# Kernel tuning notes

Hardware: AMD Instinct MI355X
Metric: run time of the kernel (lower is better)

Reference implementation:

```python
import jax, jax.numpy as jnp
import numpy as np
from jax import lax

B, C, NH, H, W = 2, 64, 8, 256, 256
HID = int(C * 2.66)  # 170, GDFN hidden channels


def conv1x1(x, w):
    # x: [b,c,h,w], w: [o,c] (1x1 conv, no bias)
    return jnp.einsum('bchw,oc->bohw', x, w)


def dwconv3(x, w):
    # depthwise 3x3, SAME padding; w: [ch,1,3,3]
    return lax.conv_general_dilated(
        x, w, window_strides=(1, 1), padding='SAME',
        feature_group_count=x.shape[1],
        dimension_numbers=('NCHW', 'OIHW', 'NCHW'))


def ln_ch(x, w, b, eps=1e-5):
    # LayerNorm over channel dim (torch does LN on [b,hw,c] then transposes back)
    mu = jnp.mean(x, axis=1, keepdims=True)
    var = jnp.mean((x - mu) ** 2, axis=1, keepdims=True)
    return (x - mu) / jnp.sqrt(var + eps) * w[None, :, None, None] + b[None, :, None, None]


def l2norm(x, eps=1e-12):
    # F.normalize(dim=-1): x / max(||x||_2, eps)
    n = jnp.sqrt(jnp.sum(x * x, axis=-1, keepdims=True))
    return x / jnp.maximum(n, eps)


def setup_inputs() -> dict:
    key = jax.random.key(0)
    ks = jax.random.split(key, 8)
    s = 0.02
    return dict(
        x=jax.random.normal(ks[0], (B, C, H, W), jnp.float32),
        y=jax.random.normal(ks[1], (B, C, H, W), jnp.float32),
        ln11_w=jnp.ones((C,), jnp.float32), ln11_b=jnp.zeros((C,), jnp.float32),
        ln12_w=jnp.ones((C,), jnp.float32), ln12_b=jnp.zeros((C,), jnp.float32),
        ln2_w=jnp.ones((C,), jnp.float32), ln2_b=jnp.zeros((C,), jnp.float32),
        qkv_w=jax.random.normal(ks[2], (3 * C, C), jnp.float32) * s,
        qkv_dw=jax.random.normal(ks[3], (3 * C, 1, 3, 3), jnp.float32) * s,
        temperature=jnp.ones((1, NH, 1, 1), jnp.float32),
        gdfn_in_w=jax.random.normal(ks[4], (2 * HID, C), jnp.float32) * s,
        gdfn_dw=jax.random.normal(ks[5], (2 * HID, 1, 3, 3), jnp.float32) * s,
        gdfn_out_w=jax.random.normal(ks[6], (C, HID), jnp.float32) * s,
    )


def _block(x, y, ln11_w, ln11_b, ln12_w, ln12_b, ln2_w, ln2_b,
           qkv_w, qkv_dw, temperature, gdfn_in_w, gdfn_dw, gdfn_out_w):
    b, c, h, w = x.shape
    xn = ln_ch(x, ln11_w, ln11_b)
    yn = ln_ch(y, ln12_w, ln12_b)

    def qkv_heads(z):
        t = dwconv3(conv1x1(z, qkv_w), qkv_dw)
        q, k, v = jnp.split(t, 3, axis=1)
        r = lambda a: a.reshape(b, NH, c // NH, h * w)
        return r(q), r(k), r(v)

    q, k, v = qkv_heads(xn)
    q1, k1, v1 = qkv_heads(yn)
    q, k, q1, k1 = l2norm(q), l2norm(k), l2norm(q1), l2norm(k1)

    # channel attention: [b,nh,c/nh,c/nh]; only cross_feature is used by the block
    attn_du = jax.nn.softmax(jnp.einsum('bhcn,bhdn->bhcd', q1, k) * temperature, axis=-1)
    attn_ud = jax.nn.softmax(jnp.einsum('bhcn,bhdn->bhcd', q, k1) * temperature, axis=-1)
    cross = (jnp.einsum('bhcd,bhdn->bhcn', attn_du, v) +
             jnp.einsum('bhcd,bhdn->bhcn', attn_ud, v1)).reshape(b, c, h, w)

    x = x + cross

    # GDFN
    xn2 = ln_ch(x, ln2_w, ln2_b)
    t = dwconv3(conv1x1(xn2, gdfn_in_w), gdfn_dw)
    x1, x2 = jnp.split(t, 2, axis=1)
    x = x + conv1x1(jax.nn.gelu(x1, approximate=False) * x2, gdfn_out_w)
    return x


def reference(x, y, ln11_w, ln11_b, ln12_w, ln12_b, ln2_w, ln2_b,
              qkv_w, qkv_dw, temperature, gdfn_in_w, gdfn_dw, gdfn_out_w):
    return _block(x, y, ln11_w, ln11_b, ln12_w, ln12_b, ln2_w, ln2_b,
                  qkv_w, qkv_dw, temperature, gdfn_in_w, gdfn_dw, gdfn_out_w)
```

## Files before the change

### kernel.cpp

```cpp
#include <hip/hip_runtime.h>
#include <hip/hip_bf16.h>
#include <math.h>

#define HWn 65536
#define Hh 256
#define Wd 256
#define Bb 2
#define Cc 64
#define NHh 8
#define HIDc 170
#define PXN 131072

typedef __hip_bfloat16 bf16;
typedef __attribute__((ext_vector_type(8))) short short8;
typedef __attribute__((ext_vector_type(4))) short s16x4;
typedef __attribute__((ext_vector_type(4))) float f32x4;

__device__ inline float b2f(short u) {
    unsigned int x = ((unsigned int)(unsigned short)u) << 16;
    return __uint_as_float(x);
}
__device__ inline short f2b(float f) {
    __hip_bfloat16 h = __float2bfloat16(f);
    return *reinterpret_cast<short*>(&h);
}
__device__ __forceinline__ void zero8(short8& v) {
#pragma unroll
    for (int e = 0; e < 8; e++) v[e] = 0;
}
__device__ __forceinline__ float rfl(float x) {
    return __uint_as_float(__builtin_amdgcn_readfirstlane(__float_as_uint(x)));
}
__device__ __forceinline__ float gelu_f(float x) {
    float z = fabsf(x) * 0.70710678118654752f;
    float tt = __builtin_amdgcn_rcpf(fmaf(0.3275911f, z, 1.f));
    float p = tt * fmaf(tt, fmaf(tt, fmaf(tt, fmaf(tt, 1.061405429f, -1.453152027f),
                                          1.421413741f), -0.284496736f), 0.254829592f);
    float e = __expf(-z * z);
    float er = fmaf(-p, e, 1.f);
    er = copysignf(er, x);
    return 0.5f * x * (1.f + er);
}

__device__ __forceinline__ void dw_row_f(const bf16* __restrict__ base, int y, int t,
                                         const float* wv, float acc[8]) {
#pragma unroll
    for (int e = 0; e < 8; e++) acc[e] = 0.f;
#pragma unroll
    for (int dy = 0; dy < 3; dy++) {
        int ys = y + dy - 1;
        if (ys < 0 || ys >= 256) continue;
        const bf16* rp = base + (size_t)ys * 2048 + (size_t)t * 8;
        short8 c8 = *reinterpret_cast<const short8*>(rp);
        short8 l8, r8;
        if (t > 0) l8 = *reinterpret_cast<const short8*>(rp - 8); else zero8(l8);
        if (t < 255) r8 = *reinterpret_cast<const short8*>(rp + 8); else zero8(r8);
#pragma unroll
        for (int e = 0; e < 8; e++)
            acc[e] += wv[e * 9 + dy * 3] * b2f(l8[e]) +
                      wv[e * 9 + dy * 3 + 1] * b2f(c8[e]) +
                      wv[e * 9 + dy * 3 + 2] * b2f(r8[e]);
    }
}

__global__ void zero_k(float* p, int n) {
    for (int i = threadIdx.x; i < n; i += 256) p[i] = 0.f;
}

__global__ __launch_bounds__(256, 2)
void ln_px(const float* __restrict__ x, const float* __restrict__ y,
           const float* __restrict__ w1, const float* __restrict__ b1,
           const float* __restrict__ w2, const float* __restrict__ b2,
           bf16* __restrict__ outx, bf16* __restrict__ outy) {
    const float* src = blockIdx.y ? y : x;
    const float* w = blockIdx.y ? w2 : w1;
    const float* bia = blockIdx.y ? b2 : b1;
    bf16* out = blockIdx.y ? outy : outx;
    int idx = blockIdx.x * 256 + threadIdx.x;
    int b = idx >> 16, p = idx & 65535;
    const float* xp = src + (size_t)b * 64 * HWn + p;
    float f[64];
    float s = 0.f;
#pragma unroll
    for (int c = 0; c < 64; c++) { f[c] = xp[(size_t)c * HWn]; s += f[c]; }
    float mu = s * (1.f / 64.f);
    float s2 = 0.f;
#pragma unroll
    for (int c = 0; c < 64; c++) { float d = f[c] - mu; s2 += d * d; }
    float inv = rsqrtf(s2 * (1.f / 64.f) + 1e-5f);
#pragma unroll
    for (int c8 = 0; c8 < 8; c8++) {
        short8 o;
#pragma unroll
        for (int e = 0; e < 8; e++) {
            int c = c8 * 8 + e;
            o[e] = f2b((f[c] - mu) * inv * w[c] + bia[c]);
        }
        *reinterpret_cast<short8*>(out + ((size_t)c8 * PXN + idx) * 8) = o;
    }
}

__global__ __launch_bounds__(256)
void conv1x1_mfma(const bf16* __restrict__ inA, const bf16* __restrict__ inB,
                  const float* __restrict__ w, int nstrips, int remap,
                  bf16* __restrict__ outA, bf16* __restrict__ outB) {
    const bf16* in = blockIdx.y ? inB : inA;
    bf16* out = blockIdx.y ? outB : outA;
    int lane = threadIdx.x & 63, wid = threadIdx.x >> 6;
    int r16 = lane & 15, grp = lane >> 4;
    size_t px0 = (size_t)blockIdx.x * 64;
    const bf16* bp0 = in + ((size_t)grp * PXN + px0 + r16) * 8;
    const bf16* bp1 = in + (((size_t)grp + 4) * PXN + px0 + r16) * 8;
    short8 b0[4], b1[4];
#pragma unroll
    for (int s = 0; s < 4; s++) {
        b0[s] = *reinterpret_cast<const short8*>(bp0 + s * 128);
        b1[s] = *reinterpret_cast<const short8*>(bp1 + s * 128);
    }
    for (int si = wid; si < nstrips; si += 4) {
        int co = si * 16 + r16;
        int row = co;
        if (remap) row = co < 170 ? co : (co >= 176 && co < 346 ? co - 6 : -1);
        short8 a0, a1;
        if (row >= 0) {
            const float* wr = w + (size_t)row * 64 + grp * 8;
#pragma unroll
            for (int e = 0; e < 8; e++) { a0[e] = f2b(wr[e]); a1[e] = f2b(wr[32 + e]); }
        } else {
            zero8(a0); zero8(a1);
        }
        int ochunk = si * 2 + (grp >> 1);
        int osub = (grp & 1) * 4;
#pragma unroll
        for (int s = 0; s < 4; s++) {
            f32x4 acc = {0.f, 0.f, 0.f, 0.f};
            acc = __builtin_amdgcn_mfma_f32_16x16x32_bf16(a0, b0[s], acc, 0, 0, 0);
            acc = __builtin_amdgcn_mfma_f32_16x16x32_bf16(a1, b1[s], acc, 0, 0, 0);
            size_t px = px0 + s * 16 + r16;
            s16x4 o;
#pragma unroll
            for (int j = 0; j < 4; j++) o[j] = f2b(acc[j]);
            *reinterpret_cast<s16x4*>(out + ((size_t)ochunk * PXN + px) * 8 + osub) = o;
        }
    }
}

__global__ __launch_bounds__(256, 4)
void dwconv_span(const bf16* __restrict__ inx, const bf16* __restrict__ iny,
                 const float* __restrict__ w, int c0,
                 bf16* __restrict__ outx, bf16* __restrict__ outy) {
    int cid = blockIdx.x >> 7;
    int rb = blockIdx.x & 127;
    int chunk = c0 + cid;
    const bf16* in = blockIdx.y ? iny : inx;
    bf16* out = blockIdx.y ? outy : outx;
    int t = threadIdx.x;
    float wv[72];
#pragma unroll
    for (int i = 0; i < 72; i++) wv[i] = w[chunk * 72 + i];
    int b = rb >> 6;
    const bf16* base = in + ((size_t)chunk * PXN + (size_t)b * 65536) * 8;
    bf16* obase = out + ((size_t)cid * PXN + (size_t)b * 65536) * 8;
#pragma unroll
    for (int r = 0; r < 4; r++) {
        int y = (rb * 4 + r) & 255;
        float acc[8];
        dw_row_f(base, y, t, wv, acc);
        short8 o;
#pragma unroll
        for (int e = 0; e < 8; e++) o[e] = f2b(acc[e]);
        *reinterpret_cast<short8*>(obase + ((size_t)y * 256 + t) * 8) = o;
    }
}

__global__ __launch_bounds__(256, 2)
void attn_dots_px(const bf16* __restrict__ qkx, const bf16* __restrict__ qky,
                  float* __restrict__ G, float* __restrict__ NA,
                  float* __restrict__ NB) {
    int which = blockIdx.z;
    int bh = blockIdx.y;
    int b = bh >> 3, h = bh & 7;
    const bf16* Aq = (which == 0 ? qky : qkx) + ((size_t)h * PXN + (size_t)b * 65536) * 8;
    const bf16* Bk = (which == 0 ? qkx : qky) + (((size_t)8 + h) * PXN + (size_t)b * 65536) * 8;
    float acc[8][8], na[8], nb[8];
#pragma unroll
    for (int c = 0; c < 8; c++) {
        na[c] = 0.f; nb[c] = 0.f;
#pragma unroll
        for (int d = 0; d < 8; d++) acc[c][d] = 0.f;
    }
    int per = 65536 / gridDim.x;
    int n0 = blockIdx.x * per;
    for (int n = n0 + threadIdx.x; n < n0 + per; n += 256) {
        short8 q8 = *reinterpret_cast<const short8*>(Aq + (size_t)n * 8);
        short8 k8 = *reinterpret_cast<const short8*>(Bk + (size_t)n * 8);
        float av[8], bv[8];
#pragma unroll
        for (int i = 0; i < 8; i++) { av[i] = b2f(q8[i]); bv[i] = b2f(k8[i]); }
#pragma unroll
        for (int c = 0; c < 8; c++) na[c] = fmaf(av[c], av[c], na[c]);
#pragma unroll
        for (int d = 0; d < 8; d++) nb[d] = fmaf(bv[d], bv[d], nb[d]);
#pragma unroll
        for (int c = 0; c < 8; c++)
#pragma unroll
            for (int d = 0; d < 8; d++) acc[c][d] = fmaf(av[c], bv[d], acc[c][d]);
    }
    size_t gbase = (((size_t)which * Bb + b) * 8 + h);
    float* Gp = G + gbase * 64;
#pragma unroll
    for (int c = 0; c < 8; c++)
#pragma unroll
        for (int d = 0; d < 8; d++) {
            float s = acc[c][d];
#pragma unroll
            for (int m = 1; m < 64; m <<= 1) s += __shfl_xor(s, m);
            if ((threadIdx.x & 63) == 0) atomicAdd(&Gp[c * 8 + d], s);
        }
#pragma unroll
    for (int c = 0; c < 8; c++) {
        float s = na[c];
#pragma unroll
        for (int m = 1; m < 64; m <<= 1) s += __shfl_xor(s, m);
        if ((threadIdx.x & 63) == 0) atomicAdd(&NA[gbase * 8 + c], s);
        float s2 = nb[c];
#pragma unroll
        for (int m = 1; m < 64; m <<= 1) s2 += __shfl_xor(s2, m);
        if ((threadIdx.x & 63) == 0) atomicAdd(&NB[gbase * 8 + c], s2);
    }
}

__global__ __launch_bounds__(256, 2)
void cross_ln2_px(const float* __restrict__ x, const bf16* __restrict__ vx,
                  const bf16* __restrict__ vy, const float* __restrict__ G,
                  const float* __restrict__ NA, const float* __restrict__ NB,
                  const float* __restrict__ temp,
                  const float* __restrict__ ln2w, const float* __restrict__ ln2b,
                  float* __restrict__ out, bf16* __restrict__ xn2) {
    int idx = blockIdx.x * 256 + threadIdx.x;
    int b = idx >> 16, p = idx & 65535;
    __shared__ float a1[512], a2[512];
    int t = threadIdx.x;
    if (t < 128) {
        int which = t >> 6, h = (t >> 3) & 7, c = t & 7;
        size_t gbase = (((size_t)which * Bb + b) * 8 + h);
        const float* Gp = G + gbase * 64 + c * 8;
        float an = fmaxf(sqrtf(NA[gbase * 8 + c]), 1e-12f);
        float tm = temp[h];
        float vals[8];
        float mx = -1e30f;
#pragma unroll
        for (int d = 0; d < 8; d++) {
            float bn = fmaxf(sqrtf(NB[gbase * 8 + d]), 1e-12f);
            float v = Gp[d] / (an * bn) * tm;
            vals[d] = v;
            mx = fmaxf(mx, v);
        }
        float se = 0.f;
#pragma unroll
        for (int d = 0; d < 8; d++) { vals[d] = expf(vals[d] - mx); se += vals[d]; }
        float inv = 1.f / se;
        float* ap = (which ? a2 : a1) + h * 64 + c * 8;
#pragma unroll
        for (int d = 0; d < 8; d++) ap[d] = vals[d] * inv;
    }
    __syncthreads();
    float o[64];
    const float* xp = x + (size_t)b * 64 * HWn + p;
#pragma unroll
    for (int c = 0; c < 64; c++) o[c] = xp[(size_t)c * HWn];
#pragma unroll
    for (int h = 0; h < 8; h++) {
        short8 v8 = *reinterpret_cast<const short8*>(vx + ((size_t)h * PXN + idx) * 8);
        short8 w8 = *reinterpret_cast<const short8*>(vy + ((size_t)h * PXN + idx) * 8);
        float v[8], v1[8];
#pragma unroll
        for (int d = 0; d < 8; d++) { v[d] = b2f(v8[d]); v1[d] = b2f(w8[d]); }
#pragma unroll
        for (int ci = 0; ci < 8; ci++) {
            float s = 0.f;
            const float* r1 = a1 + h * 64 + ci * 8;
            const float* r2 = a2 + h * 64 + ci * 8;
#pragma unroll
            for (int d = 0; d < 8; d++) s += r1[d] * v[d] + r2[d] * v1[d];
            o[h * 8 + ci] += s;
        }
    }
    float* op = out + (size_t)b * 64 * HWn + p;
    float s = 0.f;
#pragma unroll
    for (int c = 0; c < 64; c++) { op[(size_t)c * HWn] = o[c]; s += o[c]; }
    float mu = s * (1.f / 64.f);
    float s2 = 0.f;
#pragma unroll
    for (int c = 0; c < 64; c++) { float d = o[c] - mu; s2 += d * d; }
    float inv = rsqrtf(s2 * (1.f / 64.f) + 1e-5f);
#pragma unroll
    for (int c8 = 0; c8 < 8; c8++) {
        short8 o8;
#pragma unroll
        for (int e = 0; e < 8; e++) {
            int c = c8 * 8 + e;
            o8[e] = f2b((o[c] - mu) * inv * ln2w[c] + ln2b[c]);
        }
        *reinterpret_cast<short8*>(xn2 + ((size_t)c8 * PXN + idx) * 8) = o8;
    }
}

__global__ __launch_bounds__(256, 3)
void dwconv_gate(const bf16* __restrict__ g, const float* __restrict__ w,
                 bf16* __restrict__ tout) {
    int c = blockIdx.x >> 7;
    int rb = blockIdx.x & 127;
    int t = threadIdx.x;
    int b = rb >> 6;
    float wv[72];
#pragma unroll
    for (int i = 0; i < 72; i++)
        wv[i] = (c * 8 + i / 9 < 170) ? rfl(w[c * 72 + i]) : 0.f;
    const bf16* base1 = g + ((size_t)c * PXN + (size_t)b * 65536) * 8;
    float a1r[4][8];
#pragma unroll
    for (int r = 0; r < 4; r++) {
        int y = (rb * 4 + r) & 255;
        dw_row_f(base1, y, t, wv, a1r[r]);
    }
#pragma unroll
    for (int i = 0; i < 72; i++)
        wv[i] = (c * 8 + i / 9 < 170) ? rfl(w[(170 + c * 8) * 9 + i]) : 0.f;
    const bf16* base2 = g + (((size_t)22 + c) * PXN + (size_t)b * 65536) * 8;
    bf16* obase = tout + ((size_t)c * PXN + (size_t)b * 65536) * 8;
#pragma unroll
    for (int r = 0; r < 4; r++) {
        int y = (rb * 4 + r) & 255;
        float a2[8];
        dw_row_f(base2, y, t, wv, a2);
        short8 o;
#pragma unroll
        for (int e = 0; e < 8; e++)
            o[e] = f2b(gelu_f(a1r[r][e]) * a2[e]);
        *reinterpret_cast<short8*>(obase + ((size_t)y * 256 + t) * 8) = o;
    }
}

__global__ __launch_bounds__(256, 4)
void gdfn_out_mfma(const bf16* __restrict__ t, const float* __restrict__ wout,
                   float* __restrict__ out) {
    int lane = threadIdx.x & 63, wid = threadIdx.x >> 6;
    int r16 = lane & 15, grp = lane >> 4;
    size_t px0 = (size_t)blockIdx.x * 64;
    int co = wid * 16 + r16;
    short8 af[6];
#pragma unroll
    for (int kc = 0; kc < 6; kc++) {
#pragma unroll
        for (int e = 0; e < 8; e++) {
            int k = kc * 32 + grp * 8 + e;
            af[kc][e] = (k < 170) ? f2b(wout[(size_t)co * 170 + k]) : (short)0;
        }
    }
#pragma unroll
    for (int s = 0; s < 4; s++) {
        size_t px = px0 + s * 16 + r16;
        f32x4 acc = {0.f, 0.f, 0.f, 0.f};
#pragma unroll
        for (int kc = 0; kc < 6; kc++) {
            int cidx = kc * 4 + grp;
            short8 bv;
            if (cidx < 22) bv = *reinterpret_cast<const short8*>(t + ((size_t)cidx * PXN + px) * 8);
            else zero8(bv);
            acc = __builtin_amdgcn_mfma_f32_16x16x32_bf16(af[kc], bv, acc, 0, 0, 0);
        }
        int b = (int)(px >> 16);
        int p = (int)(px & 65535);
        float* op = out + (size_t)b * 64 * HWn + (size_t)(wid * 16 + grp * 4) * HWn + p;
#pragma unroll
        for (int j = 0; j < 4; j++) op[(size_t)j * HWn] += acc[j];
    }
}

extern "C" void kernel_launch(void* const* d_in, const int* in_sizes, int n_in,
                              void* d_out, int out_size, void* d_ws, size_t ws_size,
                              hipStream_t stream) {
    const float* x = (const float*)d_in[0];
    const float* y = (const float*)d_in[1];
    const float* ln11_w = (const float*)d_in[2];
    const float* ln11_b = (const float*)d_in[3];
    const float* ln12_w = (const float*)d_in[4];
    const float* ln12_b = (const float*)d_in[5];
    const float* ln2_w = (const float*)d_in[6];
    const float* ln2_b = (const float*)d_in[7];
    const float* qkv_w = (const float*)d_in[8];
    const float* qkv_dw = (const float*)d_in[9];
    const float* temp = (const float*)d_in[10];
    const float* gdfn_in_w = (const float*)d_in[11];
    const float* gdfn_dw = (const float*)d_in[12];
    const float* gdfn_out_w = (const float*)d_in[13];
    float* out = (float*)d_out;

    char* wsb = (char*)d_ws;
    float* G = (float*)wsb;
    float* NA = G + 2048;
    float* NB = NA + 256;
    bf16* hp = (bf16*)(wsb + 18944);
    bf16* xn   = hp;
    bf16* yn   = hp + (size_t)8388608;
    bf16* qkx  = hp;
    bf16* tx   = hp + (size_t)16777216;
    bf16* ty   = hp + (size_t)41943040;
    bf16* qky  = hp + (size_t)67108864;
    bf16* vx   = hp + (size_t)83886080;
    bf16* vy   = hp + (size_t)92274688;
    bf16* g    = hp + (size_t)16777216;
    bf16* t    = hp + (size_t)67108864;
    bf16* xn2  = hp;

    zero_k<<<1, 256, 0, stream>>>(G, 2560);

    ln_px<<<dim3(512, 2), 256, 0, stream>>>(x, y, ln11_w, ln11_b, ln12_w, ln12_b, xn, yn);

    conv1x1_mfma<<<dim3(2048, 2), 256, 0, stream>>>(xn, yn, qkv_w, 12, 0, tx, ty);

    dwconv_span<<<dim3(16 * 128, 2), 256, 0, stream>>>(tx, ty, qkv_dw, 0, qkx, qky);
    dwconv_span<<<dim3(8 * 128, 2), 256, 0, stream>>>(tx, ty, qkv_dw, 16, vx, vy);

    attn_dots_px<<<dim3(16, 16, 2), 256, 0, stream>>>(qkx, qky, G, NA, NB);

    cross_ln2_px<<<512, 256, 0, stream>>>(x, vx, vy, G, NA, NB, temp, ln2_w, ln2_b, out, xn2);

    conv1x1_mfma<<<dim3(2048, 1), 256, 0, stream>>>(xn2, xn2, gdfn_in_w, 22, 1, g, g);
    dwconv_gate<<<22 * 128, 256, 0, stream>>>(g, gdfn_dw, t);
    gdfn_out_mfma<<<2048, 256, 0, stream>>>(t, gdfn_out_w, out);
}
```

Before: 306.5 us.

## Store residual as bf16 and pack dwconv math into float2 ops

The residual after cross attention is now written as bf16 in the blocked channel layout instead of fp32 NCHW to the output, and the final GDFN projection reads it back and writes the output once rather than doing a read-modify-write. The depthwise convolutions unpack bf16 pairs into float2 vectors so the compiler can use packed FMA, and the two qkv dwconv launches are merged into one. This cuts fp32 residual traffic and instruction count, but rounds the residual to bf16, which may reduce accuracy.

```diff
diff --git a/kernel.cpp b/kernel.cpp
--- a/kernel.cpp
+++ b/kernel.cpp
@@ -15,6 +15,8 @@
 typedef __attribute__((ext_vector_type(8))) short short8;
 typedef __attribute__((ext_vector_type(4))) short s16x4;
 typedef __attribute__((ext_vector_type(4))) float f32x4;
+typedef __attribute__((ext_vector_type(2))) float f32x2;
+typedef __attribute__((ext_vector_type(4))) unsigned int u32x4;
 
 __device__ inline float b2f(short u) {
     unsigned int x = ((unsigned int)(unsigned short)u) << 16;
@@ -30,6 +32,12 @@
 }
 __device__ __forceinline__ float rfl(float x) {
     return __uint_as_float(__builtin_amdgcn_readfirstlane(__float_as_uint(x)));
+}
+__device__ __forceinline__ f32x2 bp2f(unsigned int d) {
+    f32x2 r;
+    r.x = __uint_as_float(d << 16);
+    r.y = __uint_as_float(d & 0xffff0000u);
+    return r;
 }
 __device__ __forceinline__ float gelu_f(float x) {
     float z = fabsf(x) * 0.70710678118654752f;
@@ -42,24 +50,30 @@
     return 0.5f * x * (1.f + er);
 }
 
-__device__ __forceinline__ void dw_row_f(const bf16* __restrict__ base, int y, int t,
-                                         const float* wv, float acc[8]) {
-#pragma unroll
-    for (int e = 0; e < 8; e++) acc[e] = 0.f;
+__device__ __forceinline__ void dw_row_p(const bf16* __restrict__ base, int y, int t,
+                                         const f32x2* wp, f32x2 acc[4]) {
+#pragma unroll
+    for (int p = 0; p < 4; p++) { acc[p].x = 0.f; acc[p].y = 0.f; }
 #pragma unroll
     for (int dy = 0; dy < 3; dy++) {
         int ys = y + dy - 1;
         if (ys < 0 || ys >= 256) continue;
         const bf16* rp = base + (size_t)ys * 2048 + (size_t)t * 8;
-        short8 c8 = *reinterpret_cast<const short8*>(rp);
-        short8 l8, r8;
-        if (t > 0) l8 = *reinterpret_cast<const short8*>(rp - 8); else zero8(l8);
-        if (t < 255) r8 = *reinterpret_cast<const short8*>(rp + 8); else zero8(r8);
-#pragma unroll
-        for (int e = 0; e < 8; e++)
-            acc[e] += wv[e * 9 + dy * 3] * b2f(l8[e]) +
-                      wv[e * 9 + dy * 3 + 1] * b2f(c8[e]) +
-                      wv[e * 9 + dy * 3 + 2] * b2f(r8[e]);
+        u32x4 c4 = *reinterpret_cast<const u32x4*>(rp);
+        u32x4 l4, r4;
+        if (t > 0) l4 = *reinterpret_cast<const u32x4*>(rp - 8);
+        else { l4.x = 0; l4.y = 0; l4.z = 0; l4.w = 0; }
+        if (t < 255) r4 = *reinterpret_cast<const u32x4*>(rp + 8);
+        else { r4.x = 0; r4.y = 0; r4.z = 0; r4.w = 0; }
+#pragma unroll
+        for (int p = 0; p < 4; p++) {
+            f32x2 fl = bp2f(l4[p]);
+            f32x2 fc = bp2f(c4[p]);
+            f32x2 fr = bp2f(r4[p]);
+            acc[p] += wp[(dy * 3 + 0) * 4 + p] * fl;
+            acc[p] += wp[(dy * 3 + 1) * 4 + p] * fc;
+            acc[p] += wp[(dy * 3 + 2) * 4 + p] * fr;
+        }
     }
 }
 
@@ -147,28 +161,36 @@
 
 __global__ __launch_bounds__(256, 4)
 void dwconv_span(const bf16* __restrict__ inx, const bf16* __restrict__ iny,
-                 const float* __restrict__ w, int c0,
-                 bf16* __restrict__ outx, bf16* __restrict__ outy) {
+                 const float* __restrict__ w,
+                 bf16* __restrict__ qkx, bf16* __restrict__ qky,
+                 bf16* __restrict__ vx, bf16* __restrict__ vy) {
     int cid = blockIdx.x >> 7;
     int rb = blockIdx.x & 127;
-    int chunk = c0 + cid;
     const bf16* in = blockIdx.y ? iny : inx;
-    bf16* out = blockIdx.y ? outy : outx;
+    bf16* out;
+    int oc;
+    if (cid < 16) { out = blockIdx.y ? qky : qkx; oc = cid; }
+    else          { out = blockIdx.y ? vy : vx;   oc = cid - 16; }
     int t = threadIdx.x;
-    float wv[72];
-#pragma unroll
-    for (int i = 0; i < 72; i++) wv[i] = w[chunk * 72 + i];
+    f32x2 wp[36];
+#pragma unroll
+    for (int k = 0; k < 9; k++)
+#pragma unroll
+        for (int p = 0; p < 4; p++) {
+            wp[k * 4 + p].x = w[cid * 72 + (2 * p) * 9 + k];
+            wp[k * 4 + p].y = w[cid * 72 + (2 * p + 1) * 9 + k];
+        }
     int b = rb >> 6;
-    const bf16* base = in + ((size_t)chunk * PXN + (size_t)b * 65536) * 8;
-    bf16* obase = out + ((size_t)cid * PXN + (size_t)b * 65536) * 8;
+    const bf16* base = in + ((size_t)cid * PXN + (size_t)b * 65536) * 8;
+    bf16* obase = out + ((size_t)oc * PXN + (size_t)b * 65536) * 8;
 #pragma unroll
     for (int r = 0; r < 4; r++) {
         int y = (rb * 4 + r) & 255;
-        float acc[8];
-        dw_row_f(base, y, t, wv, acc);
+        f32x2 acc[4];
+        dw_row_p(base, y, t, wp, acc);
         short8 o;
 #pragma unroll
-        for (int e = 0; e < 8; e++) o[e] = f2b(acc[e]);
+        for (int p = 0; p < 4; p++) { o[2 * p] = f2b(acc[p].x); o[2 * p + 1] = f2b(acc[p].y); }
         *reinterpret_cast<short8*>(obase + ((size_t)y * 256 + t) * 8) = o;
     }
 }
@@ -236,7 +258,7 @@
                   const float* __restrict__ NA, const float* __restrict__ NB,
                   const float* __restrict__ temp,
                   const float* __restrict__ ln2w, const float* __restrict__ ln2b,
-                  float* __restrict__ out, bf16* __restrict__ xn2) {
+                  bf16* __restrict__ res, bf16* __restrict__ xn2) {
     int idx = blockIdx.x * 256 + threadIdx.x;
     int b = idx >> 16, p = idx & 65535;
     __shared__ float a1[512], a2[512];
@@ -286,10 +308,9 @@
             o[h * 8 + ci] += s;
         }
     }
-    float* op = out + (size_t)b * 64 * HWn + p;
     float s = 0.f;
 #pragma unroll
-    for (int c = 0; c < 64; c++) { op[(size_t)c * HWn] = o[c]; s += o[c]; }
+    for (int c = 0; c < 64; c++) s += o[c];
     float mu = s * (1.f / 64.f);
     float s2 = 0.f;
 #pragma unroll
@@ -297,12 +318,14 @@
     float inv = rsqrtf(s2 * (1.f / 64.f) + 1e-5f);
 #pragma unroll
     for (int c8 = 0; c8 < 8; c8++) {
-        short8 o8;
+        short8 r8v, o8;
 #pragma unroll
         for (int e = 0; e < 8; e++) {
             int c = c8 * 8 + e;
+            r8v[e] = f2b(o[c]);
             o8[e] = f2b((o[c] - mu) * inv * ln2w[c] + ln2b[c]);
         }
+        *reinterpret_cast<short8*>(res + ((size_t)c8 * PXN + idx) * 8) = r8v;
         *reinterpret_cast<short8*>(xn2 + ((size_t)c8 * PXN + idx) * 8) = o8;
     }
 }
@@ -314,38 +337,50 @@
     int rb = blockIdx.x & 127;
     int t = threadIdx.x;
     int b = rb >> 6;
-    float wv[72];
-#pragma unroll
-    for (int i = 0; i < 72; i++)
-        wv[i] = (c * 8 + i / 9 < 170) ? rfl(w[c * 72 + i]) : 0.f;
+    f32x2 wp[36];
+#pragma unroll
+    for (int k = 0; k < 9; k++)
+#pragma unroll
+        for (int p = 0; p < 4; p++) {
+            int ch0 = c * 8 + 2 * p, ch1 = ch0 + 1;
+            wp[k * 4 + p].x = (ch0 < 170) ? rfl(w[ch0 * 9 + k]) : 0.f;
+            wp[k * 4 + p].y = (ch1 < 170) ? rfl(w[ch1 * 9 + k]) : 0.f;
+        }
     const bf16* base1 = g + ((size_t)c * PXN + (size_t)b * 65536) * 8;
-    float a1r[4][8];
+    f32x2 a1r[4][4];
 #pragma unroll
     for (int r = 0; r < 4; r++) {
         int y = (rb * 4 + r) & 255;
-        dw_row_f(base1, y, t, wv, a1r[r]);
-    }
-#pragma unroll
-    for (int i = 0; i < 72; i++)
-        wv[i] = (c * 8 + i / 9 < 170) ? rfl(w[(170 + c * 8) * 9 + i]) : 0.f;
+        dw_row_p(base1, y, t, wp, a1r[r]);
+    }
+#pragma unroll
+    for (int k = 0; k < 9; k++)
+#pragma unroll
+        for (int p = 0; p < 4; p++) {
+            int ch0 = c * 8 + 2 * p, ch1 = ch0 + 1;
+            wp[k * 4 + p].x = (ch0 < 170) ? rfl(w[(170 + ch0) * 9 + k]) : 0.f;
+            wp[k * 4 + p].y = (ch1 < 170) ? rfl(w[(170 + ch1) * 9 + k]) : 0.f;
+        }
     const bf16* base2 = g + (((size_t)22 + c) * PXN + (size_t)b * 65536) * 8;
     bf16* obase = tout + ((size_t)c * PXN + (size_t)b * 65536) * 8;
 #pragma unroll
     for (int r = 0; r < 4; r++) {
         int y = (rb * 4 + r) & 255;
-        float a2[8];
-        dw_row_f(base2, y, t, wv, a2);
+        f32x2 a2[4];
+        dw_row_p(base2, y, t, wp, a2);
         short8 o;
 #pragma unroll
-        for (int e = 0; e < 8; e++)
-            o[e] = f2b(gelu_f(a1r[r][e]) * a2[e]);
+        for (int p = 0; p < 4; p++) {
+            o[2 * p]     = f2b(gelu_f(a1r[r][p].x) * a2[p].x);
+            o[2 * p + 1] = f2b(gelu_f(a1r[r][p].y) * a2[p].y);
+        }
         *reinterpret_cast<short8*>(obase + ((size_t)y * 256 + t) * 8) = o;
     }
 }
 
 __global__ __launch_bounds__(256, 4)
-void gdfn_out_mfma(const bf16* __restrict__ t, const float* __restrict__ wout,
-                   float* __restrict__ out) {
+void gdfn_out_mfma(const bf16* __restrict__ t, const bf16* __restrict__ res,
+                   const float* __restrict__ wout, float* __restrict__ out) {
     int lane = threadIdx.x & 63, wid = threadIdx.x >> 6;
     int r16 = lane & 15, grp = lane >> 4;
     size_t px0 = (size_t)blockIdx.x * 64;
@@ -359,6 +394,8 @@
             af[kc][e] = (k < 170) ? f2b(wout[(size_t)co * 170 + k]) : (short)0;
         }
     }
+    int rchunk = wid * 2 + (grp >> 1);
+    int rsub = (grp & 1) * 4;
 #pragma unroll
     for (int s = 0; s < 4; s++) {
         size_t px = px0 + s * 16 + r16;
@@ -371,11 +408,12 @@
             else zero8(bv);
             acc = __builtin_amdgcn_mfma_f32_16x16x32_bf16(af[kc], bv, acc, 0, 0, 0);
         }
+        s16x4 rv = *reinterpret_cast<const s16x4*>(res + ((size_t)rchunk * PXN + px) * 8 + rsub);
         int b = (int)(px >> 16);
         int p = (int)(px & 65535);
         float* op = out + (size_t)b * 64 * HWn + (size_t)(wid * 16 + grp * 4) * HWn + p;
 #pragma unroll
-        for (int j = 0; j < 4; j++) op[(size_t)j * HWn] += acc[j];
+        for (int j = 0; j < 4; j++) op[(size_t)j * HWn] = b2f(rv[j]) + acc[j];
     }
 }
 
@@ -414,6 +452,7 @@
     bf16* g    = hp + (size_t)16777216;
     bf16* t    = hp + (size_t)67108864;
     bf16* xn2  = hp;
+    bf16* res  = hp + (size_t)8388608;
 
     zero_k<<<1, 256, 0, stream>>>(G, 2560);
 
@@ -421,14 +460,13 @@
 
     conv1x1_mfma<<<dim3(2048, 2), 256, 0, stream>>>(xn, yn, qkv_w, 12, 0, tx, ty);
 
-    dwconv_span<<<dim3(16 * 128, 2), 256, 0, stream>>>(tx, ty, qkv_dw, 0, qkx, qky);
-    dwconv_span<<<dim3(8 * 128, 2), 256, 0, stream>>>(tx, ty, qkv_dw, 16, vx, vy);
+    dwconv_span<<<dim3(24 * 128, 2), 256, 0, stream>>>(tx, ty, qkv_dw, qkx, qky, vx, vy);
 
     attn_dots_px<<<dim3(16, 16, 2), 256, 0, stream>>>(qkx, qky, G, NA, NB);
 
-    cross_ln2_px<<<512, 256, 0, stream>>>(x, vx, vy, G, NA, NB, temp, ln2_w, ln2_b, out, xn2);
+    cross_ln2_px<<<512, 256, 0, stream>>>(x, vx, vy, G, NA, NB, temp, ln2_w, ln2_b, res, xn2);
 
     conv1x1_mfma<<<dim3(2048, 1), 256, 0, stream>>>(xn2, xn2, gdfn_in_w, 22, 1, g, g);
     dwconv_gate<<<22 * 128, 256, 0, stream>>>(g, gdfn_dw, t);
-    gdfn_out_mfma<<<2048, 256, 0, stream>>>(t, gdfn_out_w, out);
-}
+    gdfn_out_mfma<<<2048, 256, 0, stream>>>(t, res, gdfn_out_w, out);
+}
```

After: 285.7 us. 6.8% less time.
